# Kernel optimization log

Hardware: AMD Instinct MI355X
Metric: run time of the kernel (lower is better)

## Reference

```python
import jax, jax.numpy as jnp
import numpy as np

N_NODES = 100000
N_EDGES = 1200000
N_GRAPHS = 512
IN_DIM, HID, N_CLS = 16, 64, 2
EPS = 1e-5


def setup_inputs() -> dict:
    key = jax.random.key(0)
    ks = jax.random.split(key, 24)
    d = {}
    d["x"] = jax.random.normal(ks[0], (N_NODES, IN_DIM), dtype=jnp.float32)
    d["edge_index"] = jax.random.randint(ks[1], (2, N_EDGES), 0, N_NODES, dtype=jnp.int32)
    d["batch_ids"] = jnp.sort(jax.random.randint(ks[2], (N_NODES,), 0, N_GRAPHS, dtype=jnp.int32))
    # input batchnorm affine
    d["bn_in_g"] = jnp.ones((IN_DIM,), jnp.float32)
    d["bn_in_b"] = jnp.zeros((IN_DIM,), jnp.float32)
    # 3 GCN layers: weight, bias, bn gamma, bn beta
    dims = [(IN_DIM, HID), (HID, HID), (HID, HID)]
    for i, (ci, co) in enumerate(dims):
        s = 1.0 / np.sqrt(ci)
        d[f"W{i}"] = jax.random.uniform(ks[3 + 4 * i], (ci, co), jnp.float32, -s, s)
        d[f"b{i}"] = jnp.zeros((co,), jnp.float32)
        d[f"g{i}"] = jnp.ones((co,), jnp.float32)
        d[f"be{i}"] = jnp.zeros((co,), jnp.float32)
    # classifier head: Linear(HID,HID) -> ReLU -> Linear(HID,N_CLS)
    s = 1.0 / np.sqrt(HID)
    d["Wc1"] = jax.random.uniform(ks[20], (HID, HID), jnp.float32, -s, s)
    d["bc1"] = jax.random.uniform(ks[21], (HID,), jnp.float32, -s, s)
    d["Wc2"] = jax.random.uniform(ks[22], (HID, N_CLS), jnp.float32, -s, s)
    d["bc2"] = jax.random.uniform(ks[23], (N_CLS,), jnp.float32, -s, s)
    return d


def _batchnorm(x, g, b):
    # training-mode BatchNorm1d: biased batch stats over nodes
    m = jnp.mean(x, axis=0)
    v = jnp.mean(jnp.square(x - m), axis=0)
    return (x - m) * jax.lax.rsqrt(v + EPS) * g + b


def _gcn(x, W, b, src, dst, dis):
    # GCNConv: out[i] = sum_{j->i} dis[j]*dis[i] * (x_j W) + b  (self-loops included in src/dst)
    h = x @ W                                  # [N, co]
    msg = h[src] * (dis[src] * dis[dst])[:, None]  # [E+N, co] gather
    return jax.ops.segment_sum(msg, dst, num_segments=N_NODES) + b


def reference(x, bn_in_g, bn_in_b, W0, b0, g0, be0, W1, b1, g1, be1,
              W2, b2, g2, be2, Wc1, bc1, Wc2, bc2, edge_index, batch_ids):
    loops = jnp.arange(N_NODES, dtype=edge_index.dtype)
    src = jnp.concatenate([edge_index[0], loops])
    dst = jnp.concatenate([edge_index[1], loops])
    deg = jax.ops.segment_sum(jnp.ones(src.shape[0], x.dtype), dst, num_segments=N_NODES)
    dis = jnp.where(deg > 0, jax.lax.rsqrt(jnp.maximum(deg, 1e-12)), 0.0)

    h = _batchnorm(x, bn_in_g, bn_in_b)
    for W, b, g, be in ((W0, b0, g0, be0), (W1, b1, g1, be1), (W2, b2, g2, be2)):
        h = jax.nn.relu(_batchnorm(_gcn(h, W, b, src, dst, dis), g, be))

    # global mean pool over graphs
    sums = jax.ops.segment_sum(h, batch_ids, num_segments=N_GRAPHS)
    cnt = jax.ops.segment_sum(jnp.ones((N_NODES,), h.dtype), batch_ids, num_segments=N_GRAPHS)
    pooled = sums / jnp.maximum(cnt, 1.0)[:, None]

    # classifier head (dropout omitted: eval mode)
    z = jax.nn.relu(pooled @ Wc1 + bc1)
    return z @ Wc2 + bc2
```

## Files before the change

kernel.cpp:

```cpp
#include <hip/hip_runtime.h>
#include <hip/hip_bf16.h>

#define N_NODES 100000
#define N_EDGES 1200000
#define N_GRAPHS 512
#define HID 64
#define IN_DIM 16
#define EPS 1e-5f

#define NB_BUCKETS 391
#define BUCKET_SPAN 256
#define REGION 4096
#define BIN_TILE 4096
#define CSR_LEN (N_EDGES + N_NODES)
#define NREP 64

typedef _Float16 half4 __attribute__((ext_vector_type(4)));
typedef _Float16 half8 __attribute__((ext_vector_type(8)));


__global__ void bin_kernel(const int* __restrict__ ei, int* __restrict__ bucketCnt,
                           int* __restrict__ regions) {
    __shared__ int hist[NB_BUCKETS], basem[NB_BUCKETS], cur[NB_BUCKETS];
    int t = threadIdx.x;
    for (int i = t; i < NB_BUCKETS; i += 256) { hist[i] = 0; cur[i] = 0; }
    __syncthreads();
    const int4* ei4s = (const int4*)ei;
    const int4* ei4d = (const int4*)(ei + N_EDGES);
    int srcs[16], dsts[16];
#pragma unroll
    for (int i = 0; i < 4; i++) {
        int idx4 = blockIdx.x * (BIN_TILE / 4) + t + i * 256;
        if (idx4 * 4 < N_EDGES) {
            int4 s4 = ei4s[idx4];
            int4 d4 = ei4d[idx4];
            srcs[i * 4 + 0] = s4.x; dsts[i * 4 + 0] = d4.x;
            srcs[i * 4 + 1] = s4.y; dsts[i * 4 + 1] = d4.y;
            srcs[i * 4 + 2] = s4.z; dsts[i * 4 + 2] = d4.z;
            srcs[i * 4 + 3] = s4.w; dsts[i * 4 + 3] = d4.w;
            atomicAdd(&hist[d4.x >> 8], 1);
            atomicAdd(&hist[d4.y >> 8], 1);
            atomicAdd(&hist[d4.z >> 8], 1);
            atomicAdd(&hist[d4.w >> 8], 1);
        } else {
            dsts[i * 4 + 0] = -1; dsts[i * 4 + 1] = -1;
            dsts[i * 4 + 2] = -1; dsts[i * 4 + 3] = -1;
        }
    }
    __syncthreads();
    for (int i = t; i < NB_BUCKETS; i += 256) {
        int h = hist[i];
        basem[i] = h ? atomicAdd(&bucketCnt[i], h) : 0;
    }
    __syncthreads();
#pragma unroll
    for (int i = 0; i < 16; i++) {
        if (dsts[i] >= 0) {
            int b = dsts[i] >> 8;
            int pos = basem[b] + atomicAdd(&cur[b], 1);
            if (pos < REGION)
                regions[b * REGION + pos] = srcs[i] | ((dsts[i] & 255) << 17);
        }
    }
}

__global__ void build_kernel(const int* __restrict__ regions, const int* __restrict__ bucketCnt,
                             int* __restrict__ csrOff, int* __restrict__ csrSrc,
                             float* __restrict__ dis) {
    __shared__ int deg[256], off[256], cur[256];
    __shared__ int slice[REGION + 256];
    __shared__ int sTot, sBase;
    int b = blockIdx.x, t = threadIdx.x;
    {
        int s = 0;
        for (int i = t; i < NB_BUCKETS; i += 256)
            if (i < b) s += min(bucketCnt[i], REGION);
        deg[t] = s;
        __syncthreads();
        for (int k = 128; k > 0; k >>= 1) {
            if (t < k) deg[t] += deg[t + k];
            __syncthreads();
        }
        if (t == 0) sBase = deg[0] + b * BUCKET_SPAN;
        __syncthreads();
    }
    int bb = sBase;
    int cnt = min(bucketCnt[b], REGION);
    int nbase = b * BUCKET_SPAN;
    int n = nbase + t;
    bool valid = (n < N_NODES);
    deg[t] = valid ? 1 : 0;
    __syncthreads();
    for (int i = t; i < cnt; i += 256) {
        int rec = regions[b * REGION + i];
        atomicAdd(&deg[rec >> 17], 1);
    }
    __syncthreads();
    int d = deg[t];
    off[t] = d;
    __syncthreads();
    for (int s = 1; s < 256; s <<= 1) {
        int v = (t >= s) ? off[t - s] : 0;
        __syncthreads();
        off[t] += v;
        __syncthreads();
    }
    int excl = off[t] - d;
    if (valid) {
        csrOff[n] = bb + excl;
        dis[n] = rsqrtf((float)d);
    }
    if (b == 0 && t == 0) csrOff[N_NODES] = CSR_LEN;
    if (t == 255) sTot = off[255];
    cur[t] = excl;
    __syncthreads();
    if (valid) {
        int pos = atomicAdd(&cur[t], 1);
        slice[pos] = n;
    }
    for (int i = t; i < cnt; i += 256) {
        int rec = regions[b * REGION + i];
        int pos = atomicAdd(&cur[rec >> 17], 1);
        slice[pos] = rec & 0x1FFFF;
    }
    __syncthreads();
    int tot = sTot;
    for (int i = t; i < tot; i += 256) csrSrc[bb + i] = slice[i];
}


__global__ void stats_x(const float* __restrict__ x, float* __restrict__ sums,
                        float* __restrict__ sumsq, _Float16* __restrict__ hwBuf) {
    __shared__ float ls[16], lq[16];
    int t = threadIdx.x;
    if (blockIdx.x == 0 && t < 8)
        ((float4*)(hwBuf + (size_t)N_NODES * HID))[t] = make_float4(0.f, 0.f, 0.f, 0.f);
    if (t < 16) { ls[t] = 0.f; lq[t] = 0.f; }
    __syncthreads();
    float s = 0.f, q = 0.f;
    const int total = N_NODES * IN_DIM;
    for (int i = blockIdx.x * blockDim.x + t; i < total; i += gridDim.x * blockDim.x) {
        float v = x[i];
        s += v; q += v * v;
    }
    int k = t & 15;
    atomicAdd(&ls[k], s);
    atomicAdd(&lq[k], q);
    __syncthreads();
    if (t < 16) { atomicAdd(&sums[t], ls[t]); atomicAdd(&sumsq[t], lq[t]); }
}

__device__ __forceinline__ void bn_coef(const float* sums, const float* sumsq,
                                        const float* gamma, const float* beta, int k,
                                        float& sc, float& sh) {
    const float invn = 1.0f / (float)N_NODES;
    float m = sums[k] * invn;
    float var = sumsq[k] * invn - m * m;
    float rs = rsqrtf(var + EPS);
    sc = gamma[k] * rs;
    sh = beta[k] - m * sc;
}

__device__ __forceinline__ void bn_coef_rep(const float* rep, const float* gamma,
                                            const float* beta, int k, float& sc, float& sh) {
    float S = 0.f, Q = 0.f;
    for (int r = 0; r < NREP; r++) { S += rep[r * 128 + k]; Q += rep[r * 128 + 64 + k]; }
    const float invn = 1.0f / (float)N_NODES;
    float m = S * invn;
    float var = Q * invn - m * m;
    float rs = rsqrtf(var + EPS);
    sc = gamma[k] * rs;
    sh = beta[k] - m * sc;
}


__global__ void premsg_kernel(const float* __restrict__ x, const float* __restrict__ sums,
                              const float* __restrict__ sumsq, const float* __restrict__ gamma,
                              const float* __restrict__ beta, const float* __restrict__ dis,
                              half4* __restrict__ m4) {
    __shared__ float sc16[16], sh16[16];
    int t = threadIdx.x;
    if (t < 16) bn_coef(sums, sumsq, gamma, beta, t, sc16[t], sh16[t]);
    __syncthreads();
    int idx = blockIdx.x * 256 + t;
    if (idx < (N_NODES + 1) * 4) {
        int n = idx >> 2, c = idx & 3;
        half4 o;
        o.x = (_Float16)0.f; o.y = (_Float16)0.f; o.z = (_Float16)0.f; o.w = (_Float16)0.f;
        if (n < N_NODES) {
            float4 h = ((const float4*)x)[idx];
            float d = dis[n];
            o.x = (_Float16)((h.x * sc16[c * 4 + 0] + sh16[c * 4 + 0]) * d);
            o.y = (_Float16)((h.y * sc16[c * 4 + 1] + sh16[c * 4 + 1]) * d);
            o.z = (_Float16)((h.z * sc16[c * 4 + 2] + sh16[c * 4 + 2]) * d);
            o.w = (_Float16)((h.w * sc16[c * 4 + 3] + sh16[c * 4 + 3]) * d);
        }
        m4[idx] = o;
    }
}

__global__ void agg16_gemm0_kernel(const half4* __restrict__ m4, const int* __restrict__ csrOff,
                                   const int* __restrict__ csrSrc, const float* __restrict__ dis,
                                   const float* __restrict__ W, const float* __restrict__ bias,
                                   _Float16* __restrict__ y, float* __restrict__ statsRep) {
    const int t = threadIdx.x;
    const int lane = t & 63;
    const int wid = t >> 6;
    const int g = lane >> 4;
    const int s = lane & 15;
    const int fl = s & 3;
    const int q = s >> 2;
    const int wave = blockIdx.x * 4 + wid;
    const int nwaves = gridDim.x * 4;

    float wreg[16][4];
#pragma unroll
    for (int k = 0; k < 16; k++) {
#pragma unroll
        for (int j = 0; j < 4; j++) wreg[k][j] = W[k * HID + s + 16 * j];
    }
    float bj[4];
#pragma unroll
    for (int j = 0; j < 4; j++) bj[j] = bias[s + 16 * j];
    float sv[4] = {0.f, 0.f, 0.f, 0.f}, qv[4] = {0.f, 0.f, 0.f, 0.f};

    for (int n0 = wave * 4; n0 < N_NODES; n0 += nwaves * 4) {
        int n = n0 + g;
        bool vn = (n < N_NODES);
        int beg = 0, end = 0;
        if (vn) { beg = csrOff[n]; end = csrOff[n + 1]; }
        float4 acc = make_float4(0.f, 0.f, 0.f, 0.f);
        int e = beg + q;
        int i0 = (e < end) ? csrSrc[e] : N_NODES;
        int i1 = (e + 4 < end) ? csrSrc[e + 4] : N_NODES;
        while (e < end) {
            int j0 = i0, j1 = i1;
            e += 8;
            i0 = (e < end) ? csrSrc[e] : N_NODES;
            i1 = (e + 4 < end) ? csrSrc[e + 4] : N_NODES;
            half4 v0 = m4[(size_t)j0 * 4 + fl];
            half4 v1 = m4[(size_t)j1 * 4 + fl];
            acc.x += (float)v0.x + (float)v1.x;
            acc.y += (float)v0.y + (float)v1.y;
            acc.z += (float)v0.z + (float)v1.z;
            acc.w += (float)v0.w + (float)v1.w;
        }
        acc.x += __shfl_xor(acc.x, 4, 64);  acc.y += __shfl_xor(acc.y, 4, 64);
        acc.z += __shfl_xor(acc.z, 4, 64);  acc.w += __shfl_xor(acc.w, 4, 64);
        acc.x += __shfl_xor(acc.x, 8, 64);  acc.y += __shfl_xor(acc.y, 8, 64);
        acc.z += __shfl_xor(acc.z, 8, 64);  acc.w += __shfl_xor(acc.w, 8, 64);
        float d = vn ? dis[n] : 0.f;
        acc.x *= d; acc.y *= d; acc.z *= d; acc.w *= d;
        float yv0 = bj[0], yv1 = bj[1], yv2 = bj[2], yv3 = bj[3];
        const int gbase = lane & 48;
#pragma unroll
        for (int k = 0; k < 16; k++) {
            float comp = ((k & 3) == 0) ? acc.x : ((k & 3) == 1) ? acc.y
                        : ((k & 3) == 2) ? acc.z : acc.w;
            float a = __shfl(comp, gbase + (k >> 2), 64);
            yv0 += a * wreg[k][0];
            yv1 += a * wreg[k][1];
            yv2 += a * wreg[k][2];
            yv3 += a * wreg[k][3];
        }
        if (vn) {
            _Float16* yr = y + (size_t)n * HID;
            yr[s] = (_Float16)yv0; yr[s + 16] = (_Float16)yv1;
            yr[s + 32] = (_Float16)yv2; yr[s + 48] = (_Float16)yv3;
            sv[0] += yv0; qv[0] += yv0 * yv0;
            sv[1] += yv1; qv[1] += yv1 * yv1;
            sv[2] += yv2; qv[2] += yv2 * yv2;
            sv[3] += yv3; qv[3] += yv3 * yv3;
        }
    }
#pragma unroll
    for (int j = 0; j < 4; j++) {
        sv[j] += __shfl_xor(sv[j], 16, 64); sv[j] += __shfl_xor(sv[j], 32, 64);
        qv[j] += __shfl_xor(qv[j], 16, 64); qv[j] += __shfl_xor(qv[j], 32, 64);
    }
    __shared__ float ls[4][64], lq[4][64];
    if (g == 0) {
#pragma unroll
        for (int j = 0; j < 4; j++) { ls[wid][s + 16 * j] = sv[j]; lq[wid][s + 16 * j] = qv[j]; }
    }
    __syncthreads();
    if (wid == 0) {
        float S = ls[0][lane] + ls[1][lane] + ls[2][lane] + ls[3][lane];
        float Q = lq[0][lane] + lq[1][lane] + lq[2][lane] + lq[3][lane];
        float* rep = statsRep + (blockIdx.x & (NREP - 1)) * 128;
        atomicAdd(&rep[lane], S);
        atomicAdd(&rep[64 + lane], Q);
    }
}


#define G64_ROWS 128
__global__ void gemm64_kernel(const _Float16* __restrict__ hin, const float* __restrict__ W,
                              const float* __restrict__ statsRep, const float* __restrict__ gamma,
                              const float* __restrict__ beta, const float* __restrict__ dis,
                              _Float16* __restrict__ hout) {
    __shared__ float Ws[HID * HID];
    __shared__ float hs[G64_ROWS][HID + 2];
    __shared__ float scb[64], shb[64];
    int t = threadIdx.x;
    int fg = t & 15;
    int rg = t >> 4;
    int base = blockIdx.x * G64_ROWS;

    if (t < 64) bn_coef_rep(statsRep, gamma, beta, t, scb[t], shb[t]);
    {
        const float4* W4 = (const float4*)W;
        float4* Ws4 = (float4*)Ws;
        for (int i = t; i < HID * HID / 4; i += 256) Ws4[i] = W4[i];
    }
    __syncthreads();
    {
        const half4* hin4 = (const half4*)hin;
        for (int i = t; i < G64_ROWS * 16; i += 256) {
            int r = i >> 4, c = i & 15;
            int n = base + r;
            float4 v = make_float4(0.f, 0.f, 0.f, 0.f);
            if (n < N_NODES) {
                half4 h = hin4[n * 16 + c];
                v.x = fmaxf((float)h.x * scb[c * 4 + 0] + shb[c * 4 + 0], 0.f);
                v.y = fmaxf((float)h.y * scb[c * 4 + 1] + shb[c * 4 + 1], 0.f);
                v.z = fmaxf((float)h.z * scb[c * 4 + 2] + shb[c * 4 + 2], 0.f);
                v.w = fmaxf((float)h.w * scb[c * 4 + 3] + shb[c * 4 + 3], 0.f);
            }
            hs[r][c * 4 + 0] = v.x;
            hs[r][c * 4 + 1] = v.y;
            hs[r][c * 4 + 2] = v.z;
            hs[r][c * 4 + 3] = v.w;
        }
    }
    __syncthreads();

    float4 acc[8];
#pragma unroll
    for (int r = 0; r < 8; r++) acc[r] = make_float4(0.f, 0.f, 0.f, 0.f);
    const float4* Ws4 = (const float4*)Ws;
    for (int k = 0; k < HID; k += 2) {
        float4 wk0 = Ws4[k * 16 + fg];
        float4 wk1 = Ws4[(k + 1) * 16 + fg];
#pragma unroll
        for (int r = 0; r < 8; r++) {
            float2 h2 = *(const float2*)&hs[rg * 8 + r][k];
            acc[r].x += h2.x * wk0.x + h2.y * wk1.x;
            acc[r].y += h2.x * wk0.y + h2.y * wk1.y;
            acc[r].z += h2.x * wk0.z + h2.y * wk1.z;
            acc[r].w += h2.x * wk0.w + h2.y * wk1.w;
        }
    }
    half4* hout4 = (half4*)hout;
#pragma unroll
    for (int r = 0; r < 8; r++) {
        int n = base + rg * 8 + r;
        if (n < N_NODES) {
            float dsc = dis[n];
            half4 o;
            o.x = (_Float16)(acc[r].x * dsc);
            o.y = (_Float16)(acc[r].y * dsc);
            o.z = (_Float16)(acc[r].z * dsc);
            o.w = (_Float16)(acc[r].w * dsc);
            hout4[n * 16 + fg] = o;
        }
    }
}


__global__ void aggregate_kernel(const half8* __restrict__ hwh, const int* __restrict__ csrOff,
                                 const int* __restrict__ csrSrc, const float* __restrict__ dis,
                                 const float* __restrict__ bias, half8* __restrict__ y8,
                                 float* __restrict__ statsRep) {
    const int lane = threadIdx.x & 63;
    const int wid = threadIdx.x >> 6;
    const int g = lane >> 5;
    const int s = lane & 31;
    const int c = s & 7;
    const int o = s >> 3;
    const int wave = blockIdx.x * 4 + wid;
    const int nwaves = gridDim.x * 4;

    const float4 bv0 = ((const float4*)bias)[c * 2];
    const float4 bv1 = ((const float4*)bias)[c * 2 + 1];
    float sa[8], qa[8];
#pragma unroll
    for (int j = 0; j < 8; j++) { sa[j] = 0.f; qa[j] = 0.f; }

    for (int n0 = wave * 2; n0 < N_NODES; n0 += nwaves * 2) {
        int n = n0 + g;
        bool vn = (n < N_NODES);
        int beg = 0, end = 0;
        if (vn) { beg = csrOff[n]; end = csrOff[n + 1]; }
        float acc[8];
#pragma unroll
        for (int j = 0; j < 8; j++) acc[j] = 0.f;
        int e = beg + o;
        int i0 = (e < end) ? csrSrc[e] : N_NODES;
        int i1 = (e + 4 < end) ? csrSrc[e + 4] : N_NODES;
        while (e < end) {
            int j0 = i0, j1 = i1;
            e += 8;
            i0 = (e < end) ? csrSrc[e] : N_NODES;
            i1 = (e + 4 < end) ? csrSrc[e + 4] : N_NODES;
            half8 h0 = hwh[(size_t)j0 * 8 + c];
            half8 h1 = hwh[(size_t)j1 * 8 + c];
#pragma unroll
            for (int j = 0; j < 8; j++) acc[j] += (float)h0[j] + (float)h1[j];
        }
#pragma unroll
        for (int j = 0; j < 8; j++) {
            acc[j] += __shfl_xor(acc[j], 8, 64);
            acc[j] += __shfl_xor(acc[j], 16, 64);
        }
        if (o == 0 && vn) {
            float d = dis[n];
            float val[8];
            val[0] = acc[0] * d + bv0.x; val[1] = acc[1] * d + bv0.y;
            val[2] = acc[2] * d + bv0.z; val[3] = acc[3] * d + bv0.w;
            val[4] = acc[4] * d + bv1.x; val[5] = acc[5] * d + bv1.y;
            val[6] = acc[6] * d + bv1.z; val[7] = acc[7] * d + bv1.w;
            half8 ov;
#pragma unroll
            for (int j = 0; j < 8; j++) ov[j] = (_Float16)val[j];
            y8[(size_t)n * 8 + c] = ov;
#pragma unroll
            for (int j = 0; j < 8; j++) { sa[j] += val[j]; qa[j] += val[j] * val[j]; }
        }
    }
#pragma unroll
    for (int j = 0; j < 8; j++) {
        sa[j] += __shfl_xor(sa[j], 32, 64);
        qa[j] += __shfl_xor(qa[j], 32, 64);
    }
    __shared__ float ls[4][64], lq[4][64];
    ls[wid][lane] = 0.f;
    lq[wid][lane] = 0.f;
    if (lane < 8) {
#pragma unroll
        for (int j = 0; j < 8; j++) { ls[wid][lane * 8 + j] = sa[j]; lq[wid][lane * 8 + j] = qa[j]; }
    }
    __syncthreads();
    if (wid == 0) {
        float S = ls[0][lane] + ls[1][lane] + ls[2][lane] + ls[3][lane];
        float Q = lq[0][lane] + lq[1][lane] + lq[2][lane] + lq[3][lane];
        float* rep = statsRep + (blockIdx.x & (NREP - 1)) * 128;
        atomicAdd(&rep[lane], S);
        atomicAdd(&rep[64 + lane], Q);
    }
}


#define POOL_CHUNK 256
__global__ void pool_kernel(const _Float16* __restrict__ y, const int* __restrict__ batch,
                            const float* __restrict__ statsRep, const float* __restrict__ gamma,
                            const float* __restrict__ beta, float* __restrict__ pool,
                            float* __restrict__ cnt) {
    __shared__ float scs[64], shs[64];
    int t = threadIdx.x;
    int f = t & 63;
    int nl = t >> 6;
    if (t < 64) bn_coef_rep(statsRep, gamma, beta, t, scs[t], shs[t]);
    __syncthreads();
    float sc = scs[f], sh = shs[f];
    int base = blockIdx.x * POOL_CHUNK;
    int endn = min(base + POOL_CHUNK, N_NODES);
    int g_cur = -1;
    float acc = 0.f;
    float c_acc = 0.f;
    for (int n = base + nl; n < endn; n += 4) {
        int g = batch[n];
        float v = fmaxf((float)y[(size_t)n * HID + f] * sc + sh, 0.f);
        if (g != g_cur) {
            if (g_cur >= 0) {
                atomicAdd(&pool[g_cur * HID + f], acc);
                if (f == 0) atomicAdd(&cnt[g_cur], c_acc);
            }
            g_cur = g;
            acc = 0.f;
            c_acc = 0.f;
        }
        acc += v;
        c_acc += 1.f;
    }
    if (g_cur >= 0) {
        atomicAdd(&pool[g_cur * HID + f], acc);
        if (f == 0) atomicAdd(&cnt[g_cur], c_acc);
    }
}

__global__ void head_kernel(const float* __restrict__ pool, const float* __restrict__ cnt,
                            const float* __restrict__ Wc1, const float* __restrict__ bc1,
                            const float* __restrict__ Wc2, const float* __restrict__ bc2,
                            float* __restrict__ out) {
    int g = blockIdx.x;
    int f = threadIdx.x;
    __shared__ float p[64], z[64];
    float c = fmaxf(cnt[g], 1.0f);
    p[f] = pool[g * HID + f] / c;
    __syncthreads();
    float acc = bc1[f];
    for (int k = 0; k < 64; k++) acc += p[k] * Wc1[k * 64 + f];
    z[f] = fmaxf(acc, 0.f);
    __syncthreads();
    if (f < 2) {
        float o = bc2[f];
        for (int k = 0; k < 64; k++) o += z[k] * Wc2[k * 2 + f];
        out[g * 2 + f] = o;
    }
}


extern "C" void kernel_launch(void* const* d_in, const int* in_sizes, int n_in,
                              void* d_out, int out_size, void* d_ws, size_t ws_size,
                              hipStream_t stream) {
    const float* x      = (const float*)d_in[0];
    const int*   ei     = (const int*)d_in[1];
    const int*   batch  = (const int*)d_in[2];
    const float* bn_in_g = (const float*)d_in[3];
    const float* bn_in_b = (const float*)d_in[4];
    const float* W0 = (const float*)d_in[5];
    const float* b0 = (const float*)d_in[6];
    const float* g0 = (const float*)d_in[7];
    const float* be0 = (const float*)d_in[8];
    const float* W1 = (const float*)d_in[9];
    const float* b1 = (const float*)d_in[10];
    const float* g1 = (const float*)d_in[11];
    const float* be1 = (const float*)d_in[12];
    const float* W2 = (const float*)d_in[13];
    const float* b2 = (const float*)d_in[14];
    const float* g2 = (const float*)d_in[15];
    const float* be2 = (const float*)d_in[16];
    const float* Wc1 = (const float*)d_in[17];
    const float* bc1 = (const float*)d_in[18];
    const float* Wc2 = (const float*)d_in[19];
    const float* bc2 = (const float*)d_in[20];
    float* out = (float*)d_out;

    char* w = (char*)d_ws;
    size_t off = 0;
    auto take = [&](size_t bytes) {
        size_t r = off;
        off += (bytes + 255) & ~(size_t)255;
        return r;
    };
    float* stats    = (float*)(w + take(256 * 4));
    float* statsRep = (float*)(w + take(3 * NREP * 128 * 4));
    float* pool     = (float*)(w + take((size_t)N_GRAPHS * HID * 4));
    float* cnt      = (float*)(w + take((size_t)N_GRAPHS * 4));
    int* bucketCnt  = (int*)(w + take((size_t)NB_BUCKETS * 4));
    size_t zero_end = off;
    float* dis    = (float*)(w + take((size_t)N_NODES * 4));
    int* csrOff   = (int*)(w + take((size_t)(N_NODES + 1) * 4));
    int* csrSrc   = (int*)(w + take((size_t)(CSR_LEN + 64) * 4));
    _Float16* hwBuf = (_Float16*)(w + take((size_t)(N_NODES + 1) * HID * 2));
    _Float16* yBuf  = (_Float16*)(w + take((size_t)N_NODES * HID * 2));
    _Float16* msgBuf = (_Float16*)(w + take((size_t)(N_NODES + 1) * IN_DIM * 2));
    int* regions  = (int*)hwBuf;
    (void)ws_size; (void)n_in; (void)in_sizes; (void)out_size;

    hipMemsetAsync(w, 0, zero_end, stream);

    const int nbBin   = (N_EDGES + BIN_TILE - 1) / BIN_TILE;
    const int nbPre   = ((N_NODES + 1) * 4 + 255) / 256;
    const int nbG64   = (N_NODES + G64_ROWS - 1) / G64_ROWS;
    const int nbAgg16 = (N_NODES + 16 * 4 - 1) / (16 * 4);
    const int nbAgg64 = (N_NODES + 8 * 4 - 1) / (8 * 4);

    bin_kernel<<<nbBin, 256, 0, stream>>>(ei, bucketCnt, regions);
    build_kernel<<<NB_BUCKETS, 256, 0, stream>>>(regions, bucketCnt, csrOff, csrSrc, dis);

    float* s0 = stats;
    float* rep1 = statsRep + 0 * NREP * 128;
    float* rep2 = statsRep + 1 * NREP * 128;
    float* rep3 = statsRep + 2 * NREP * 128;

    stats_x<<<256, 256, 0, stream>>>(x, s0, s0 + 64, hwBuf);

    premsg_kernel<<<nbPre, 256, 0, stream>>>(x, s0, s0 + 64, bn_in_g, bn_in_b, dis,
                                             (half4*)msgBuf);
    agg16_gemm0_kernel<<<nbAgg16, 256, 0, stream>>>((const half4*)msgBuf, csrOff, csrSrc, dis,
                                                    W0, b0, yBuf, rep1);

    gemm64_kernel<<<nbG64, 256, 0, stream>>>(yBuf, W1, rep1, g0, be0, dis, hwBuf);
    aggregate_kernel<<<nbAgg64, 256, 0, stream>>>((const half8*)hwBuf, csrOff, csrSrc, dis, b1,
                                                  (half8*)yBuf, rep2);
    gemm64_kernel<<<nbG64, 256, 0, stream>>>(yBuf, W2, rep2, g1, be1, dis, hwBuf);
    aggregate_kernel<<<nbAgg64, 256, 0, stream>>>((const half8*)hwBuf, csrOff, csrSrc, dis, b2,
                                                  (half8*)yBuf, rep3);

    const int nbPool = (N_NODES + POOL_CHUNK - 1) / POOL_CHUNK;
    pool_kernel<<<nbPool, 256, 0, stream>>>(yBuf, batch, rep3, g2, be2, pool, cnt);
    head_kernel<<<N_GRAPHS, 64, 0, stream>>>(pool, cnt, Wc1, bc1, Wc2, bc2, out);
}
```

Baseline: 310.8 us.

## Split hidden features into 16-wide chunks so aggregation gathers stay cache-resident

Hidden activations are stored as four feature-chunk planes of 16 halfs per node instead of 64-wide rows, and aggregation launches a separate grid slice per chunk. Each chunk's gather working set is much smaller, so random neighbour reads are meant to hit cache rather than HBM. In exchange, the CSR index arrays are read four times and each gather moves only 32 bytes. GEMM, first-layer aggregation and pooling indexing are adapted to the chunked layout.

```diff
diff --git a/kernel.cpp b/kernel.cpp
--- a/kernel.cpp
+++ b/kernel.cpp
@@ -14,6 +14,11 @@
 #define BIN_TILE 4096
 #define CSR_LEN (N_EDGES + N_NODES)
 #define NREP 64
+
+#define NCHUNK 4
+#define CHUNK_ROWS ((size_t)(N_NODES + 1))
+#define CHUNK_HALFS (CHUNK_ROWS * 16)
+#define AGG_BLKS ((N_NODES + 15) / 16)
 
 typedef _Float16 half4 __attribute__((ext_vector_type(4)));
 typedef _Float16 half8 __attribute__((ext_vector_type(8)));
@@ -130,11 +135,9 @@
 
 
 __global__ void stats_x(const float* __restrict__ x, float* __restrict__ sums,
-                        float* __restrict__ sumsq, _Float16* __restrict__ hwBuf) {
+                        float* __restrict__ sumsq) {
     __shared__ float ls[16], lq[16];
     int t = threadIdx.x;
-    if (blockIdx.x == 0 && t < 8)
-        ((float4*)(hwBuf + (size_t)N_NODES * HID))[t] = make_float4(0.f, 0.f, 0.f, 0.f);
     if (t < 16) { ls[t] = 0.f; lq[t] = 0.f; }
     __syncthreads();
     float s = 0.f, q = 0.f;
@@ -264,9 +267,11 @@
             yv3 += a * wreg[k][3];
         }
         if (vn) {
-            _Float16* yr = y + (size_t)n * HID;
-            yr[s] = (_Float16)yv0; yr[s + 16] = (_Float16)yv1;
-            yr[s + 32] = (_Float16)yv2; yr[s + 48] = (_Float16)yv3;
+            _Float16* yr = y + (size_t)n * 16;
+            yr[s] = (_Float16)yv0;
+            yr[CHUNK_HALFS + s] = (_Float16)yv1;
+            yr[2 * CHUNK_HALFS + s] = (_Float16)yv2;
+            yr[3 * CHUNK_HALFS + s] = (_Float16)yv3;
             sv[0] += yv0; qv[0] += yv0 * yv0;
             sv[1] += yv1; qv[1] += yv1 * yv1;
             sv[2] += yv2; qv[2] += yv2 * yv2;
@@ -316,12 +321,13 @@
     __syncthreads();
     {
         const half4* hin4 = (const half4*)hin;
+        const size_t cs4 = CHUNK_ROWS * 4;
         for (int i = t; i < G64_ROWS * 16; i += 256) {
             int r = i >> 4, c = i & 15;
             int n = base + r;
             float4 v = make_float4(0.f, 0.f, 0.f, 0.f);
             if (n < N_NODES) {
-                half4 h = hin4[n * 16 + c];
+                half4 h = hin4[(size_t)(c >> 2) * cs4 + (size_t)n * 4 + (c & 3)];
                 v.x = fmaxf((float)h.x * scb[c * 4 + 0] + shb[c * 4 + 0], 0.f);
                 v.y = fmaxf((float)h.y * scb[c * 4 + 1] + shb[c * 4 + 1], 0.f);
                 v.z = fmaxf((float)h.z * scb[c * 4 + 2] + shb[c * 4 + 2], 0.f);
@@ -352,6 +358,8 @@
         }
     }
     half4* hout4 = (half4*)hout;
+    const size_t cs4 = CHUNK_ROWS * 4;
+    const size_t obase = (size_t)(fg >> 2) * cs4 + (size_t)(fg & 3);
 #pragma unroll
     for (int r = 0; r < 8; r++) {
         int n = base + rg * 8 + r;
@@ -362,91 +370,92 @@
             o.y = (_Float16)(acc[r].y * dsc);
             o.z = (_Float16)(acc[r].z * dsc);
             o.w = (_Float16)(acc[r].w * dsc);
-            hout4[n * 16 + fg] = o;
-        }
-    }
-}
-
-
-__global__ void aggregate_kernel(const half8* __restrict__ hwh, const int* __restrict__ csrOff,
-                                 const int* __restrict__ csrSrc, const float* __restrict__ dis,
-                                 const float* __restrict__ bias, half8* __restrict__ y8,
-                                 float* __restrict__ statsRep) {
+            hout4[obase + (size_t)n * 4] = o;
+        }
+    }
+}
+
+
+__global__ void aggregate_chunked_kernel(const half8* __restrict__ hwc,
+                                         const int* __restrict__ csrOff,
+                                         const int* __restrict__ csrSrc,
+                                         const float* __restrict__ dis,
+                                         const float* __restrict__ bias,
+                                         _Float16* __restrict__ y,
+                                         float* __restrict__ statsRep) {
     const int lane = threadIdx.x & 63;
     const int wid = threadIdx.x >> 6;
-    const int g = lane >> 5;
-    const int s = lane & 31;
-    const int c = s & 7;
-    const int o = s >> 3;
-    const int wave = blockIdx.x * 4 + wid;
-    const int nwaves = gridDim.x * 4;
-
-    const float4 bv0 = ((const float4*)bias)[c * 2];
-    const float4 bv1 = ((const float4*)bias)[c * 2 + 1];
+    const int chunk = blockIdx.x / AGG_BLKS;
+    const int blk = blockIdx.x - chunk * AGG_BLKS;
+    const int g = lane >> 4;
+    const int s = lane & 15;
+    const int c = s & 1;
+    const int slot = s >> 1;
+    const half8* hb = hwc + (size_t)chunk * (CHUNK_ROWS * 2);
+    half8* yc = (half8*)y + (size_t)chunk * (CHUNK_ROWS * 2);
+    const int f0 = chunk * 16;
+
+    float bj[8];
+#pragma unroll
+    for (int j = 0; j < 8; j++) bj[j] = bias[f0 + c * 8 + j];
     float sa[8], qa[8];
 #pragma unroll
     for (int j = 0; j < 8; j++) { sa[j] = 0.f; qa[j] = 0.f; }
 
-    for (int n0 = wave * 2; n0 < N_NODES; n0 += nwaves * 2) {
-        int n = n0 + g;
+    const int wave = blk * 4 + wid;
+    {
+        int n = wave * 4 + g;
         bool vn = (n < N_NODES);
         int beg = 0, end = 0;
         if (vn) { beg = csrOff[n]; end = csrOff[n + 1]; }
         float acc[8];
 #pragma unroll
         for (int j = 0; j < 8; j++) acc[j] = 0.f;
-        int e = beg + o;
-        int i0 = (e < end) ? csrSrc[e] : N_NODES;
-        int i1 = (e + 4 < end) ? csrSrc[e + 4] : N_NODES;
+        int e = beg + slot;
+        int i0 = (e < end) ? csrSrc[e] : 0;
         while (e < end) {
-            int j0 = i0, j1 = i1;
+            int j0 = i0;
             e += 8;
-            i0 = (e < end) ? csrSrc[e] : N_NODES;
-            i1 = (e + 4 < end) ? csrSrc[e + 4] : N_NODES;
-            half8 h0 = hwh[(size_t)j0 * 8 + c];
-            half8 h1 = hwh[(size_t)j1 * 8 + c];
-#pragma unroll
-            for (int j = 0; j < 8; j++) acc[j] += (float)h0[j] + (float)h1[j];
+            i0 = (e < end) ? csrSrc[e] : 0;
+            half8 h = hb[(size_t)j0 * 2 + c];
+#pragma unroll
+            for (int j = 0; j < 8; j++) acc[j] += (float)h[j];
         }
 #pragma unroll
         for (int j = 0; j < 8; j++) {
+            acc[j] += __shfl_xor(acc[j], 2, 64);
+            acc[j] += __shfl_xor(acc[j], 4, 64);
             acc[j] += __shfl_xor(acc[j], 8, 64);
-            acc[j] += __shfl_xor(acc[j], 16, 64);
-        }
-        if (o == 0 && vn) {
+        }
+        if (slot == 0 && vn) {
             float d = dis[n];
-            float val[8];
-            val[0] = acc[0] * d + bv0.x; val[1] = acc[1] * d + bv0.y;
-            val[2] = acc[2] * d + bv0.z; val[3] = acc[3] * d + bv0.w;
-            val[4] = acc[4] * d + bv1.x; val[5] = acc[5] * d + bv1.y;
-            val[6] = acc[6] * d + bv1.z; val[7] = acc[7] * d + bv1.w;
             half8 ov;
 #pragma unroll
-            for (int j = 0; j < 8; j++) ov[j] = (_Float16)val[j];
-            y8[(size_t)n * 8 + c] = ov;
-#pragma unroll
-            for (int j = 0; j < 8; j++) { sa[j] += val[j]; qa[j] += val[j] * val[j]; }
+            for (int j = 0; j < 8; j++) {
+                float v = acc[j] * d + bj[j];
+                ov[j] = (_Float16)v;
+                sa[j] += v; qa[j] += v * v;
+            }
+            yc[(size_t)n * 2 + c] = ov;
         }
     }
 #pragma unroll
     for (int j = 0; j < 8; j++) {
-        sa[j] += __shfl_xor(sa[j], 32, 64);
-        qa[j] += __shfl_xor(qa[j], 32, 64);
-    }
-    __shared__ float ls[4][64], lq[4][64];
-    ls[wid][lane] = 0.f;
-    lq[wid][lane] = 0.f;
-    if (lane < 8) {
+        sa[j] += __shfl_xor(sa[j], 16, 64); sa[j] += __shfl_xor(sa[j], 32, 64);
+        qa[j] += __shfl_xor(qa[j], 16, 64); qa[j] += __shfl_xor(qa[j], 32, 64);
+    }
+    __shared__ float ls[4][16], lq[4][16];
+    if (lane < 2) {
 #pragma unroll
         for (int j = 0; j < 8; j++) { ls[wid][lane * 8 + j] = sa[j]; lq[wid][lane * 8 + j] = qa[j]; }
     }
     __syncthreads();
-    if (wid == 0) {
+    if (wid == 0 && lane < 16) {
         float S = ls[0][lane] + ls[1][lane] + ls[2][lane] + ls[3][lane];
         float Q = lq[0][lane] + lq[1][lane] + lq[2][lane] + lq[3][lane];
         float* rep = statsRep + (blockIdx.x & (NREP - 1)) * 128;
-        atomicAdd(&rep[lane], S);
-        atomicAdd(&rep[64 + lane], Q);
+        atomicAdd(&rep[f0 + lane], S);
+        atomicAdd(&rep[64 + f0 + lane], Q);
     }
 }
 
@@ -463,6 +472,7 @@
     if (t < 64) bn_coef_rep(statsRep, gamma, beta, t, scs[t], shs[t]);
     __syncthreads();
     float sc = scs[f], sh = shs[f];
+    const _Float16* yf = y + (size_t)(f >> 4) * CHUNK_HALFS + (f & 15);
     int base = blockIdx.x * POOL_CHUNK;
     int endn = min(base + POOL_CHUNK, N_NODES);
     int g_cur = -1;
@@ -470,7 +480,7 @@
     float c_acc = 0.f;
     for (int n = base + nl; n < endn; n += 4) {
         int g = batch[n];
-        float v = fmaxf((float)y[(size_t)n * HID + f] * sc + sh, 0.f);
+        float v = fmaxf((float)yf[(size_t)n * 16] * sc + sh, 0.f);
         if (g != g_cur) {
             if (g_cur >= 0) {
                 atomicAdd(&pool[g_cur * HID + f], acc);
@@ -553,8 +563,8 @@
     float* dis    = (float*)(w + take((size_t)N_NODES * 4));
     int* csrOff   = (int*)(w + take((size_t)(N_NODES + 1) * 4));
     int* csrSrc   = (int*)(w + take((size_t)(CSR_LEN + 64) * 4));
-    _Float16* hwBuf = (_Float16*)(w + take((size_t)(N_NODES + 1) * HID * 2));
-    _Float16* yBuf  = (_Float16*)(w + take((size_t)N_NODES * HID * 2));
+    _Float16* hwBuf = (_Float16*)(w + take(NCHUNK * CHUNK_HALFS * 2));
+    _Float16* yBuf  = (_Float16*)(w + take(NCHUNK * CHUNK_HALFS * 2));
     _Float16* msgBuf = (_Float16*)(w + take((size_t)(N_NODES + 1) * IN_DIM * 2));
     int* regions  = (int*)hwBuf;
     (void)ws_size; (void)n_in; (void)in_sizes; (void)out_size;
@@ -565,7 +575,7 @@
     const int nbPre   = ((N_NODES + 1) * 4 + 255) / 256;
     const int nbG64   = (N_NODES + G64_ROWS - 1) / G64_ROWS;
     const int nbAgg16 = (N_NODES + 16 * 4 - 1) / (16 * 4);
-    const int nbAgg64 = (N_NODES + 8 * 4 - 1) / (8 * 4);
+    const int nbAggC  = NCHUNK * AGG_BLKS;
 
     bin_kernel<<<nbBin, 256, 0, stream>>>(ei, bucketCnt, regions);
     build_kernel<<<NB_BUCKETS, 256, 0, stream>>>(regions, bucketCnt, csrOff, csrSrc, dis);
@@ -575,7 +585,7 @@
     float* rep2 = statsRep + 1 * NREP * 128;
     float* rep3 = statsRep + 2 * NREP * 128;
 
-    stats_x<<<256, 256, 0, stream>>>(x, s0, s0 + 64, hwBuf);
+    stats_x<<<256, 256, 0, stream>>>(x, s0, s0 + 64);
 
     premsg_kernel<<<nbPre, 256, 0, stream>>>(x, s0, s0 + 64, bn_in_g, bn_in_b, dis,
                                              (half4*)msgBuf);
@@ -583,11 +593,11 @@
                                                     W0, b0, yBuf, rep1);
 
     gemm64_kernel<<<nbG64, 256, 0, stream>>>(yBuf, W1, rep1, g0, be0, dis, hwBuf);
-    aggregate_kernel<<<nbAgg64, 256, 0, stream>>>((const half8*)hwBuf, csrOff, csrSrc, dis, b1,
-                                                  (half8*)yBuf, rep2);
+    aggregate_chunked_kernel<<<nbAggC, 256, 0, stream>>>((const half8*)hwBuf, csrOff, csrSrc,
+                                                         dis, b1, yBuf, rep2);
     gemm64_kernel<<<nbG64, 256, 0, stream>>>(yBuf, W2, rep2, g1, be1, dis, hwBuf);
-    aggregate_kernel<<<nbAgg64, 256, 0, stream>>>((const half8*)hwBuf, csrOff, csrSrc, dis, b2,
-                                                  (half8*)yBuf, rep3);
+    aggregate_chunked_kernel<<<nbAggC, 256, 0, stream>>>((const half8*)hwBuf, csrOff, csrSrc,
+                                                         dis, b2, yBuf, rep3);
 
     const int nbPool = (N_NODES + POOL_CHUNK - 1) / POOL_CHUNK;
     pool_kernel<<<nbPool, 256, 0, stream>>>(yBuf, batch, rep3, g2, be2, pool, cnt);
```

Measured after the change: 393.6 us. +26.6%, slower.
